# Kernel optimization log

Measured on AMD Instinct MI355X. Metric: run time of the kernel, lower is better.

## Reference

```python
import jax, jax.numpy as jnp
import numpy as np

B, T, C, H = 4, 1024, 512, 8
HD = C // H
N_NODE, F_DIM, TOTAL_DIM = 64, 8, 16
SCALE = 1.0 / np.sqrt(HD)


def _build_mask():
    # causal tril with every (total_dim-1 mod total_dim)-th COLUMN zeroed
    m = np.tril(np.ones((T, T), dtype=np.float32))
    m[:, TOTAL_DIM - 1::TOTAL_DIM] = 0.0
    return jnp.asarray(m)

MASK = _build_mask()  # (T, T), 1 = keep, 0 = mask


def setup_inputs() -> dict:
    key = jax.random.key(0)
    ks = jax.random.split(key, 12)
    s = 0.02
    return {
        "x": jax.random.normal(ks[0], (B, T, C), dtype=jnp.float32),
        "attn_bias": jax.random.normal(ks[1], (H, N_NODE, N_NODE), dtype=jnp.float32) * 0.1,
        "Wq": jax.random.normal(ks[2], (C, C), dtype=jnp.float32) * s,
        "bq": jax.random.normal(ks[3], (C,), dtype=jnp.float32) * s,
        "Wk": jax.random.normal(ks[4], (C, C), dtype=jnp.float32) * s,
        "bk": jax.random.normal(ks[5], (C,), dtype=jnp.float32) * s,
        "Wv": jax.random.normal(ks[6], (C, C), dtype=jnp.float32) * s,
        "bv": jax.random.normal(ks[7], (C,), dtype=jnp.float32) * s,
        "Wp": jax.random.normal(ks[8], (C, C), dtype=jnp.float32) * s,
        "bp": jax.random.normal(ks[9], (C,), dtype=jnp.float32) * s,
    }


def reference(x, attn_bias, Wq, bq, Wk, bk, Wv, bv, Wp, bp):
    Bx, Tx, Cx = x.shape

    def heads(W, b):  # (B,T,C) -> (B,H,T,HD); torch Linear is x @ W.T + b
        return (x @ W.T + b).reshape(Bx, Tx, H, HD).transpose(0, 2, 1, 3)

    q, k, v = heads(Wq, bq), heads(Wk, bk), heads(Wv, bv)

    # repeat_interleave + repeat expansion == kron(attn_bias, ones(f_dim, f_dim))
    d = N_NODE * F_DIM
    bias = jnp.repeat(jnp.repeat(attn_bias, F_DIM, axis=1), F_DIM, axis=2)  # (H, d, d)
    padded_bias = jnp.zeros((H, Tx, Tx), dtype=x.dtype).at[:, :d, :d].set(bias)

    att = jnp.einsum('bhqd,bhkd->bhqk', q, k) * SCALE + padded_bias[None]
    neg = jnp.asarray(-jnp.inf, dtype=att.dtype)
    att = jnp.where(MASK[None, None, :Tx, :Tx] == 0, neg, att)
    att = jax.nn.softmax(att, axis=-1)

    y = jnp.einsum('bhqk,bhkd->bhqd', att, v)
    y = y.transpose(0, 2, 1, 3).reshape(Bx, Tx, Cx)
    return y @ Wp.T + bp
```

## Files before the change

### kernel.cpp

```cpp
#include <hip/hip_runtime.h>

#define T_SEQ 1024
#define C_DIM 512
#define H_HEADS 8
#define HDIM 64
#define B_BATCH 4
#define M_ROWS (B_BATCH * T_SEQ)
#define NSPLIT_TOT 40

typedef __attribute__((ext_vector_type(8))) short short8;
typedef __attribute__((ext_vector_type(4))) float f32x4;

__device__ __forceinline__ unsigned short f2bf(float f) {
    unsigned u = __builtin_bit_cast(unsigned, f);
    u += 0x7FFFu + ((u >> 16) & 1u);
    return (unsigned short)(u >> 16);
}

__device__ __forceinline__ float bf2f(unsigned short u) {
    return __builtin_bit_cast(float, (unsigned)u << 16);
}

__device__ __forceinline__ void gload_lds16(const unsigned short* g, unsigned short* l) {
    __builtin_amdgcn_global_load_lds(
        (const __attribute__((address_space(1))) unsigned int*)(const void*)g,
        (__attribute__((address_space(3))) unsigned int*)(void*)l, 16, 0, 0);
}

__device__ __constant__ unsigned char BX_OF[NSPLIT_TOT] =
    {0,1,2,3,4,4,5,5,6,6,7,7,8,8,8,9,9,9,10,10,10,11,11,11,
     12,12,12,12,13,13,13,13,14,14,14,14,15,15,15,15};
__device__ __constant__ unsigned char SP_OF[NSPLIT_TOT] =
    {0,0,0,0,0,1,0,1,0,1,0,1,0,1,2,0,1,2,0,1,2,0,1,2,
     0,1,2,3,0,1,2,3,0,1,2,3,0,1,2,3};
__device__ __constant__ unsigned char CUM_OF[16] =
    {0,1,2,3,4,6,8,10,12,15,18,21,24,28,32,36};

__global__ __launch_bounds__(256) void cast_all(
    const float* __restrict__ x,
    const float* __restrict__ wq, const float* __restrict__ wk,
    const float* __restrict__ wv, const float* __restrict__ wp,
    unsigned short* __restrict__ xb,
    unsigned short* __restrict__ wqb, unsigned short* __restrict__ wkb,
    unsigned short* __restrict__ wvb, unsigned short* __restrict__ wpb)
{
    const long NX = (long)M_ROWS * C_DIM;
    const long NW = (long)C_DIM * C_DIM;
    long i4 = (long)blockIdx.x * blockDim.x + threadIdx.x;
    long base = i4 * 4;
    const float* src; unsigned short* dst; long off;
    if (base < NX) { src = x; dst = xb; off = base; }
    else {
        long r = base - NX;
        int w = (int)(r >> 18);
        off = r & (NW - 1);
        switch (w) {
            case 0:  src = wq; dst = wqb; break;
            case 1:  src = wk; dst = wkb; break;
            case 2:  src = wv; dst = wvb; break;
            default: src = wp; dst = wpb; break;
        }
    }
    float4 v = *(const float4*)(src + off);
    ushort4 o;
    o.x = f2bf(v.x); o.y = f2bf(v.y); o.z = f2bf(v.z); o.w = f2bf(v.w);
    *(ushort4*)(dst + off) = o;
}

__device__ __forceinline__ void gemm_body(
    const unsigned short* __restrict__ A,
    const unsigned short* __restrict__ W,
    const float* __restrict__ bias,
    unsigned short* __restrict__ Obf,
    float* __restrict__ Of,
    int mode)
{
    __shared__ __align__(16) unsigned short Atile[2][128 * 64];
    __shared__ __align__(16) unsigned short Btile[2][64 * 64];

    const int tid  = threadIdx.x;
    const int w    = tid >> 6;
    const int lane = tid & 63;
    const int quad = lane >> 4;
    const int l16  = lane & 15;
    const int m0   = blockIdx.x * 128;
    const int n0   = blockIdx.y * 64;

    f32x4 acc[2][4] = {};

    const int lr = lane >> 3;
    const int lc = lane & 7;

    auto stage = [&](int buf, int kk) {
        for (int i = 0; i < 4; ++i) {
            int r0 = 32 * w + 8 * i;
            int r  = r0 + lr;
            int c  = lc ^ (r & 7);
            gload_lds16(&A[(long)(m0 + r) * 512 + kk + c * 8], &Atile[buf][r0 * 64]);
        }
        for (int i = 0; i < 2; ++i) {
            int r0 = 16 * w + 8 * i;
            int r  = r0 + lr;
            int c  = lc ^ (r & 7);
            gload_lds16(&W[(long)(n0 + r) * 512 + kk + c * 8], &Btile[buf][r0 * 64]);
        }
    };

    stage(0, 0);

    #pragma unroll
    for (int k0 = 0; k0 < 512; k0 += 64) {
        const int cur = (k0 >> 6) & 1;
        if (k0 + 64 < 512) {
            __builtin_amdgcn_sched_barrier(0);
            stage(cur ^ 1, k0 + 64);
            asm volatile("s_waitcnt vmcnt(6)" ::: "memory");
        } else {
            asm volatile("s_waitcnt vmcnt(0)" ::: "memory");
        }
        __builtin_amdgcn_s_barrier();
        __builtin_amdgcn_sched_barrier(0);

        for (int st = 0; st < 2; ++st) {
            const int pc = ((4 * st + quad) ^ (l16 & 7)) * 8;
            short8 af[2], bf[4];
            for (int i = 0; i < 2; ++i)
                af[i] = *(const short8*)&Atile[cur][(32 * w + 16 * i + l16) * 64 + pc];
            for (int j = 0; j < 4; ++j)
                bf[j] = *(const short8*)&Btile[cur][(16 * j + l16) * 64 + pc];
            for (int i = 0; i < 2; ++i)
                for (int j = 0; j < 4; ++j)
                    acc[i][j] = (mode == 1)
                        ? __builtin_amdgcn_mfma_f32_16x16x32_bf16(bf[j], af[i], acc[i][j], 0, 0, 0)
                        : __builtin_amdgcn_mfma_f32_16x16x32_bf16(af[i], bf[j], acc[i][j], 0, 0, 0);
        }

        __builtin_amdgcn_sched_barrier(0);
        __builtin_amdgcn_s_barrier();
    }

    if (mode == 1) {
        for (int j = 0; j < 4; ++j) {
            for (int reg = 0; reg < 4; ++reg) {
                int n = n0 + 16 * j + 4 * quad + reg;
                int h = n >> 6, hd = n & 63;
                float bv = bias[n];
                for (int i = 0; i < 2; ++i) {
                    int t = m0 + 32 * w + 16 * i + l16;
                    int b = t >> 10, tl = t & 1023;
                    Obf[(((long)(b * H_HEADS + h)) * HDIM + hd) * T_SEQ + tl] =
                        f2bf(acc[i][j][reg] + bv);
                }
            }
        }
    } else {
        for (int j = 0; j < 4; ++j) {
            int col = n0 + 16 * j + l16;
            float bv = bias[col];
            for (int i = 0; i < 2; ++i) {
                for (int reg = 0; reg < 4; ++reg) {
                    int row = m0 + 32 * w + 16 * i + 4 * quad + reg;
                    float v = acc[i][j][reg] + bv;
                    if (mode == 2) {
                        Of[(long)row * 512 + col] = v;
                    } else {
                        int b = row >> 10, t = row & 1023;
                        int h = col >> 6,  hd = col & 63;
                        Obf[(((long)(b * H_HEADS + h)) * T_SEQ + t) * HDIM + hd] = f2bf(v);
                    }
                }
            }
        }
    }
}

__global__ __launch_bounds__(256) void gemm_qkv(
    const unsigned short* __restrict__ A,
    const unsigned short* __restrict__ Wq, const unsigned short* __restrict__ Wk,
    const unsigned short* __restrict__ Wv,
    const float* __restrict__ bq, const float* __restrict__ bk, const float* __restrict__ bv,
    unsigned short* __restrict__ Q, unsigned short* __restrict__ K,
    unsigned short* __restrict__ V)
{
    const unsigned short* W; const float* b; unsigned short* O; int mode;
    if (blockIdx.z == 0)      { W = Wq; b = bq; O = Q; mode = 0; }
    else if (blockIdx.z == 1) { W = Wk; b = bk; O = K; mode = 0; }
    else                      { W = Wv; b = bv; O = V; mode = 1; }
    gemm_body(A, W, b, O, nullptr, mode);
}

__global__ __launch_bounds__(256) void gemm_out_k(
    const unsigned short* __restrict__ A, const unsigned short* __restrict__ W,
    const float* __restrict__ bias, float* __restrict__ O)
{
    gemm_body(A, W, bias, nullptr, O, 2);
}

__global__ __launch_bounds__(256, 5) void attn_split(
    const unsigned short* __restrict__ Q, const unsigned short* __restrict__ K,
    const unsigned short* __restrict__ Vt, const float* __restrict__ attn_bias,
    unsigned short* __restrict__ Opart, float* __restrict__ lpart)
{
    __shared__ __align__(16) unsigned short Kl[64 * 64];
    __shared__ __align__(16) unsigned short Vl[64 * 64];
    __shared__ __align__(16) unsigned short Pl[4][16 * 72];
    __shared__ float biasl[8][64];

    const int tid  = threadIdx.x;
    const int w    = tid >> 6;
    const int lane = tid & 63;
    const int quad = lane >> 4;
    const int l16  = lane & 15;
    const int lr   = lane >> 3;
    const int lc   = lane & 7;
    const int sidx = blockIdx.y;
    const int bh   = blockIdx.x;
    const int h    = bh & 7;
    const int bx   = BX_OF[sidx];
    const int sp   = SP_OF[sidx];
    const int q0   = bx * 64;
    const int kt0  = sp * 4;
    const int kt1  = min(kt0 + 4, bx + 1);
    const bool use_bias = (q0 < 512) && (sp < 2);

    const int qrow  = q0 + 16 * w + l16;
    const int brow2 = 2 * w + (l16 >> 3);

    if (use_bias) {
        for (int i = tid; i < 512; i += 256) {
            int nq = (q0 >> 3) + (i >> 6);
            biasl[i >> 6][i & 63] = attn_bias[h * 4096 + nq * 64 + (i & 63)];
        }
    }

    const unsigned short* Qbh = Q  + (long)bh * T_SEQ * HDIM;
    const unsigned short* Kbh = K  + (long)bh * T_SEQ * HDIM;
    const unsigned short* Vbh = Vt + (long)bh * HDIM * T_SEQ;

    short8 qf[2];
    {
        qf[0] = *(const short8*)&Qbh[(long)qrow * HDIM + 8 * quad];
        qf[1] = *(const short8*)&Qbh[(long)qrow * HDIM + 32 + 8 * quad];
    }

    f32x4 oacc[4] = {};
    float lsum = 0.f;

    for (int kt = kt0; kt < kt1; ++kt) {
        const int k0 = kt * 64;
        __syncthreads();
        for (int i = 0; i < 2; ++i) {
            int r0 = 16 * w + 8 * i;
            int r  = r0 + lr;
            int c  = lc ^ (r & 7);
            gload_lds16(&Kbh[(long)(k0 + r) * HDIM + c * 8], &Kl[r0 * 64]);
            gload_lds16(&Vbh[(long)r * T_SEQ + k0 + c * 8], &Vl[r0 * 64]);
        }
        __syncthreads();

        f32x4 s[4] = {};
        __builtin_amdgcn_s_setprio(1);
        for (int st = 0; st < 2; ++st) {
            const int pc = ((4 * st + quad) ^ (l16 & 7)) * 8;
            for (int ct = 0; ct < 4; ++ct) {
                short8 kf = *(const short8*)&Kl[(16 * ct + l16) * 64 + pc];
                s[ct] = __builtin_amdgcn_mfma_f32_16x16x32_bf16(kf, qf[st], s[ct], 0, 0, 0);
            }
        }
        __builtin_amdgcn_s_setprio(0);

        const bool diag = (kt == bx);
        #pragma unroll
        for (int ct = 0; ct < 4; ++ct) {
            const int kbase = k0 + 16 * ct + 4 * quad;
            float bval = use_bias ? biasl[brow2][(k0 >> 3) + 2 * ct + (quad >> 1)] : 0.f;
            float pv[4];
            #pragma unroll
            for (int reg = 0; reg < 4; ++reg) {
                float v = s[ct][reg] * 0.125f + bval;
                bool keep = !(quad == 3 && reg == 3);
                if (diag) keep = keep && (kbase + reg <= qrow);
                float p = keep ? __expf(v) : 0.f;
                lsum += p;
                pv[reg] = p;
            }
            uint2 d;
            d.x = (unsigned)f2bf(pv[0]) | ((unsigned)f2bf(pv[1]) << 16);
            d.y = (unsigned)f2bf(pv[2]) | ((unsigned)f2bf(pv[3]) << 16);
            *(uint2*)&Pl[w][l16 * 72 + 16 * ct + 4 * quad] = d;
        }

        __builtin_amdgcn_s_setprio(1);
        for (int st = 0; st < 2; ++st) {
            const int pc = ((4 * st + quad) ^ (l16 & 7)) * 8;
            short8 af = *(const short8*)&Pl[w][l16 * 72 + 32 * st + 8 * quad];
            for (int ct = 0; ct < 4; ++ct) {
                short8 bf = *(const short8*)&Vl[(16 * ct + l16) * 64 + pc];
                oacc[ct] = __builtin_amdgcn_mfma_f32_16x16x32_bf16(af, bf, oacc[ct], 0, 0, 0);
            }
        }
        __builtin_amdgcn_s_setprio(0);
    }

    lsum += __shfl_xor(lsum, 16);
    lsum += __shfl_xor(lsum, 32);

    const long p = (long)bh * NSPLIT_TOT + sidx;
    unsigned short* Op = Opart + p * 4096;
    for (int ct = 0; ct < 4; ++ct)
        for (int reg = 0; reg < 4; ++reg)
            Op[(16 * w + 4 * quad + reg) * 64 + 16 * ct + l16] = f2bf(oacc[ct][reg]);
    if (quad == 0)
        lpart[p * 64 + 16 * w + l16] = lsum;
}

__global__ __launch_bounds__(256) void attn_combine(
    const unsigned short* __restrict__ Opart, const float* __restrict__ lpart,
    unsigned short* __restrict__ Y)
{
    const int bx = blockIdx.y, bh = blockIdx.x;
    const int b = bh >> 3, h = bh & 7;
    const int ns = (bx >> 2) + 1;
    const long p0 = (long)bh * NSPLIT_TOT + CUM_OF[bx];
    const int tid = threadIdx.x;
    const int qr = tid >> 2;
    const int hs = (tid & 3) * 16;

    float L = 0.f;
    for (int s = 0; s < ns; ++s) L += lpart[(p0 + s) * 64 + qr];

    float acc[16] = {};
    for (int s = 0; s < ns; ++s) {
        const unsigned short* op = Opart + (p0 + s) * 4096 + qr * 64 + hs;
        short8 v0 = *(const short8*)op;
        short8 v1 = *(const short8*)(op + 8);
        for (int k = 0; k < 8; ++k) {
            acc[k]     += bf2f((unsigned short)v0[k]);
            acc[k + 8] += bf2f((unsigned short)v1[k]);
        }
    }
    float inv = 1.f / L;
    int q = bx * 64 + qr;
    unsigned short* y = Y + ((long)b * T_SEQ + q) * C_DIM + h * HDIM + hs;
    for (int j4 = 0; j4 < 4; ++j4) {
        ushort4 o;
        o.x = f2bf(acc[4 * j4 + 0] * inv); o.y = f2bf(acc[4 * j4 + 1] * inv);
        o.z = f2bf(acc[4 * j4 + 2] * inv); o.w = f2bf(acc[4 * j4 + 3] * inv);
        *(ushort4*)(y + 4 * j4) = o;
    }
}

extern "C" void kernel_launch(void* const* d_in, const int* in_sizes, int n_in,
                              void* d_out, int out_size, void* d_ws, size_t ws_size,
                              hipStream_t stream)
{
    const float* x         = (const float*)d_in[0];
    const float* attn_bias = (const float*)d_in[1];
    const float* Wq = (const float*)d_in[2]; const float* bq = (const float*)d_in[3];
    const float* Wk = (const float*)d_in[4]; const float* bk = (const float*)d_in[5];
    const float* Wv = (const float*)d_in[6]; const float* bv = (const float*)d_in[7];
    const float* Wp = (const float*)d_in[8]; const float* bp = (const float*)d_in[9];
    float* out = (float*)d_out;

    const long NX = (long)M_ROWS * C_DIM;
    const long NW = (long)C_DIM * C_DIM;

    unsigned short* xb  = (unsigned short*)d_ws;
    unsigned short* wqb = xb  + NX;
    unsigned short* wkb = wqb + NW;
    unsigned short* wvb = wkb + NW;
    unsigned short* wpb = wvb + NW;
    unsigned short* Qb  = wpb + NW;
    unsigned short* Kb  = Qb  + NX;
    unsigned short* Vtb = Kb  + NX;
    unsigned short* Yb  = Vtb + NX;
    unsigned short* Opart = Yb + NX;
    float* lpart = (float*)(Opart + (long)32 * NSPLIT_TOT * 4096);

    long n4 = (NX + 4 * NW) / 4;
    cast_all<<<dim3((unsigned)(n4 / 256)), 256, 0, stream>>>(
        x, Wq, Wk, Wv, Wp, xb, wqb, wkb, wvb, wpb);

    gemm_qkv<<<dim3(M_ROWS / 128, C_DIM / 64, 3), 256, 0, stream>>>(
        xb, wqb, wkb, wvb, bq, bk, bv, Qb, Kb, Vtb);

    attn_split<<<dim3(B_BATCH * H_HEADS, NSPLIT_TOT), 256, 0, stream>>>(
        Qb, Kb, Vtb, attn_bias, Opart, lpart);

    attn_combine<<<dim3(B_BATCH * H_HEADS, T_SEQ / 64), 256, 0, stream>>>(
        Opart, lpart, Yb);

    gemm_out_k<<<dim3(M_ROWS / 128, C_DIM / 64), 256, 0, stream>>>(
        Yb, wpb, bp, out);
}
```

Before: 122.1 us.

## Enlarge attention query tile to 128 rows to reuse K/V tiles

The split attention kernel now processes 128 query rows per block (two 16-row subtiles per wave) instead of 64. Each K/V tile loaded into LDS therefore feeds twice as many MFMAs, and there are half as many split blocks. The split table, partial-output layout and combine indexing are rewritten to match. In exchange, register and LDS use per block rise (occupancy hint drops from 5 to 4 blocks), the grid shrinks to 640 blocks, and the diagonal masking now covers two key tiles.

```diff
diff --git a/kernel.cpp b/kernel.cpp
--- a/kernel.cpp
+++ b/kernel.cpp
@@ -6,7 +6,7 @@
 #define HDIM 64
 #define B_BATCH 4
 #define M_ROWS (B_BATCH * T_SEQ)
-#define NSPLIT_TOT 40
+#define NSPLIT8 20
 
 typedef __attribute__((ext_vector_type(8))) short short8;
 typedef __attribute__((ext_vector_type(4))) float f32x4;
@@ -27,14 +27,12 @@
         (__attribute__((address_space(3))) unsigned int*)(void*)l, 16, 0, 0);
 }
 
-__device__ __constant__ unsigned char BX_OF[NSPLIT_TOT] =
-    {0,1,2,3,4,4,5,5,6,6,7,7,8,8,8,9,9,9,10,10,10,11,11,11,
-     12,12,12,12,13,13,13,13,14,14,14,14,15,15,15,15};
-__device__ __constant__ unsigned char SP_OF[NSPLIT_TOT] =
-    {0,0,0,0,0,1,0,1,0,1,0,1,0,1,2,0,1,2,0,1,2,0,1,2,
-     0,1,2,3,0,1,2,3,0,1,2,3,0,1,2,3};
-__device__ __constant__ unsigned char CUM_OF[16] =
-    {0,1,2,3,4,6,8,10,12,15,18,21,24,28,32,36};
+__device__ __constant__ unsigned char BX8_OF[NSPLIT8] =
+    {0,1,2,2,3,3,4,4,4,5,5,5,6,6,6,6,7,7,7,7};
+__device__ __constant__ unsigned char SP8_OF[NSPLIT8] =
+    {0,0,0,1,0,1,0,1,2,0,1,2,0,1,2,3,0,1,2,3};
+__device__ __constant__ unsigned char CUM8_OF[8] =
+    {0,1,2,4,6,9,12,16};
 
 __global__ __launch_bounds__(256) void cast_all(
     const float* __restrict__ x,
@@ -196,15 +194,15 @@
     gemm_body(A, W, bias, nullptr, O, 2);
 }
 
-__global__ __launch_bounds__(256, 5) void attn_split(
+__global__ __launch_bounds__(256, 4) void attn_split(
     const unsigned short* __restrict__ Q, const unsigned short* __restrict__ K,
     const unsigned short* __restrict__ Vt, const float* __restrict__ attn_bias,
     unsigned short* __restrict__ Opart, float* __restrict__ lpart)
 {
     __shared__ __align__(16) unsigned short Kl[64 * 64];
     __shared__ __align__(16) unsigned short Vl[64 * 64];
-    __shared__ __align__(16) unsigned short Pl[4][16 * 72];
-    __shared__ float biasl[8][64];
+    __shared__ __align__(16) unsigned short Pl[4][32 * 72];
+    __shared__ float biasl[16][64];
 
     const int tid  = threadIdx.x;
     const int w    = tid >> 6;
@@ -216,18 +214,16 @@
     const int sidx = blockIdx.y;
     const int bh   = blockIdx.x;
     const int h    = bh & 7;
-    const int bx   = BX_OF[sidx];
-    const int sp   = SP_OF[sidx];
-    const int q0   = bx * 64;
-    const int kt0  = sp * 4;
-    const int kt1  = min(kt0 + 4, bx + 1);
-    const bool use_bias = (q0 < 512) && (sp < 2);
-
-    const int qrow  = q0 + 16 * w + l16;
-    const int brow2 = 2 * w + (l16 >> 3);
+    const int bx8  = BX8_OF[sidx];
+    const int sp   = SP8_OF[sidx];
+    const int q0   = bx8 * 128;
+    const int nk   = 2 * bx8 + 2;
+    const int kt0  = 4 * sp;
+    const int kt1  = min(kt0 + 4, nk);
+    const bool use_bias = (bx8 < 4);
 
     if (use_bias) {
-        for (int i = tid; i < 512; i += 256) {
+        for (int i = tid; i < 1024; i += 256) {
             int nq = (q0 >> 3) + (i >> 6);
             biasl[i >> 6][i & 63] = attn_bias[h * 4096 + nq * 64 + (i & 63)];
         }
@@ -237,20 +233,23 @@
     const unsigned short* Kbh = K  + (long)bh * T_SEQ * HDIM;
     const unsigned short* Vbh = Vt + (long)bh * HDIM * T_SEQ;
 
-    short8 qf[2];
-    {
-        qf[0] = *(const short8*)&Qbh[(long)qrow * HDIM + 8 * quad];
-        qf[1] = *(const short8*)&Qbh[(long)qrow * HDIM + 32 + 8 * quad];
-    }
-
-    f32x4 oacc[4] = {};
-    float lsum = 0.f;
+    short8 qf[2][2];
+    int qrow[2];
+    #pragma unroll
+    for (int i = 0; i < 2; ++i) {
+        qrow[i] = q0 + 32 * w + 16 * i + l16;
+        qf[i][0] = *(const short8*)&Qbh[(long)qrow[i] * HDIM + 8 * quad];
+        qf[i][1] = *(const short8*)&Qbh[(long)qrow[i] * HDIM + 32 + 8 * quad];
+    }
+
+    f32x4 oacc[2][4] = {};
+    float lsum[2] = {0.f, 0.f};
 
     for (int kt = kt0; kt < kt1; ++kt) {
         const int k0 = kt * 64;
         __syncthreads();
-        for (int i = 0; i < 2; ++i) {
-            int r0 = 16 * w + 8 * i;
+        for (int i2 = 0; i2 < 2; ++i2) {
+            int r0 = 16 * w + 8 * i2;
             int r  = r0 + lr;
             int c  = lc ^ (r & 7);
             gload_lds16(&Kbh[(long)(k0 + r) * HDIM + c * 8], &Kl[r0 * 64]);
@@ -258,80 +257,104 @@
         }
         __syncthreads();
 
-        f32x4 s[4] = {};
+        f32x4 s[2][4] = {};
         __builtin_amdgcn_s_setprio(1);
         for (int st = 0; st < 2; ++st) {
             const int pc = ((4 * st + quad) ^ (l16 & 7)) * 8;
             for (int ct = 0; ct < 4; ++ct) {
                 short8 kf = *(const short8*)&Kl[(16 * ct + l16) * 64 + pc];
-                s[ct] = __builtin_amdgcn_mfma_f32_16x16x32_bf16(kf, qf[st], s[ct], 0, 0, 0);
+                s[0][ct] = __builtin_amdgcn_mfma_f32_16x16x32_bf16(kf, qf[0][st], s[0][ct], 0, 0, 0);
+                s[1][ct] = __builtin_amdgcn_mfma_f32_16x16x32_bf16(kf, qf[1][st], s[1][ct], 0, 0, 0);
             }
         }
         __builtin_amdgcn_s_setprio(0);
 
-        const bool diag = (kt == bx);
+        const bool diag = (kt >= 2 * bx8);
         #pragma unroll
-        for (int ct = 0; ct < 4; ++ct) {
-            const int kbase = k0 + 16 * ct + 4 * quad;
-            float bval = use_bias ? biasl[brow2][(k0 >> 3) + 2 * ct + (quad >> 1)] : 0.f;
-            float pv[4];
+        for (int i = 0; i < 2; ++i) {
             #pragma unroll
-            for (int reg = 0; reg < 4; ++reg) {
-                float v = s[ct][reg] * 0.125f + bval;
-                bool keep = !(quad == 3 && reg == 3);
-                if (diag) keep = keep && (kbase + reg <= qrow);
-                float p = keep ? __expf(v) : 0.f;
-                lsum += p;
-                pv[reg] = p;
+            for (int ct = 0; ct < 4; ++ct) {
+                const int kbase = k0 + 16 * ct + 4 * quad;
+                float bval = use_bias
+                    ? biasl[4 * w + 2 * i + (l16 >> 3)][(k0 >> 3) + 2 * ct + (quad >> 1)]
+                    : 0.f;
+                float pv[4];
+                #pragma unroll
+                for (int reg = 0; reg < 4; ++reg) {
+                    float v = fmaf(s[i][ct][reg], 0.125f, bval);
+                    bool keep = !(quad == 3 && reg == 3);
+                    if (diag) keep = keep && (kbase + reg <= qrow[i]);
+                    float p = keep ? __expf(v) : 0.f;
+                    lsum[i] += p;
+                    pv[reg] = p;
+                }
+                uint2 d;
+                d.x = (unsigned)f2bf(pv[0]) | ((unsigned)f2bf(pv[1]) << 16);
+                d.y = (unsigned)f2bf(pv[2]) | ((unsigned)f2bf(pv[3]) << 16);
+                *(uint2*)&Pl[w][(16 * i + l16) * 72 + 16 * ct + 4 * quad] = d;
             }
-            uint2 d;
-            d.x = (unsigned)f2bf(pv[0]) | ((unsigned)f2bf(pv[1]) << 16);
-            d.y = (unsigned)f2bf(pv[2]) | ((unsigned)f2bf(pv[3]) << 16);
-            *(uint2*)&Pl[w][l16 * 72 + 16 * ct + 4 * quad] = d;
         }
 
         __builtin_amdgcn_s_setprio(1);
         for (int st = 0; st < 2; ++st) {
             const int pc = ((4 * st + quad) ^ (l16 & 7)) * 8;
-            short8 af = *(const short8*)&Pl[w][l16 * 72 + 32 * st + 8 * quad];
-            for (int ct = 0; ct < 4; ++ct) {
-                short8 bf = *(const short8*)&Vl[(16 * ct + l16) * 64 + pc];
-                oacc[ct] = __builtin_amdgcn_mfma_f32_16x16x32_bf16(af, bf, oacc[ct], 0, 0, 0);
+            short8 vf[4];
+            #pragma unroll
+            for (int ct = 0; ct < 4; ++ct)
+                vf[ct] = *(const short8*)&Vl[(16 * ct + l16) * 64 + pc];
+            #pragma unroll
+            for (int i = 0; i < 2; ++i) {
+                short8 af = *(const short8*)&Pl[w][(16 * i + l16) * 72 + 32 * st + 8 * quad];
+                #pragma unroll
+                for (int ct = 0; ct < 4; ++ct)
+                    oacc[i][ct] = __builtin_amdgcn_mfma_f32_16x16x32_bf16(af, vf[ct], oacc[i][ct], 0, 0, 0);
             }
         }
         __builtin_amdgcn_s_setprio(0);
     }
 
-    lsum += __shfl_xor(lsum, 16);
-    lsum += __shfl_xor(lsum, 32);
-
-    const long p = (long)bh * NSPLIT_TOT + sidx;
-    unsigned short* Op = Opart + p * 4096;
-    for (int ct = 0; ct < 4; ++ct)
-        for (int reg = 0; reg < 4; ++reg)
-            Op[(16 * w + 4 * quad + reg) * 64 + 16 * ct + l16] = f2bf(oacc[ct][reg]);
-    if (quad == 0)
-        lpart[p * 64 + 16 * w + l16] = lsum;
+    #pragma unroll
+    for (int i = 0; i < 2; ++i) {
+        lsum[i] += __shfl_xor(lsum[i], 16);
+        lsum[i] += __shfl_xor(lsum[i], 32);
+    }
+
+    const long p = (long)bh * NSPLIT8 + sidx;
+    unsigned short* Op = Opart + p * 8192;
+    #pragma unroll
+    for (int i = 0; i < 2; ++i)
+        for (int ct = 0; ct < 4; ++ct)
+            for (int reg = 0; reg < 4; ++reg)
+                Op[(32 * w + 16 * i + 4 * quad + reg) * 64 + 16 * ct + l16] =
+                    f2bf(oacc[i][ct][reg]);
+    if (quad == 0) {
+        lpart[p * 128 + 32 * w + l16]      = lsum[0];
+        lpart[p * 128 + 32 * w + 16 + l16] = lsum[1];
+    }
 }
 
 __global__ __launch_bounds__(256) void attn_combine(
     const unsigned short* __restrict__ Opart, const float* __restrict__ lpart,
     unsigned short* __restrict__ Y)
 {
-    const int bx = blockIdx.y, bh = blockIdx.x;
+    const int bxc = blockIdx.y;
+    const int bh  = blockIdx.x;
     const int b = bh >> 3, h = bh & 7;
-    const int ns = (bx >> 2) + 1;
-    const long p0 = (long)bh * NSPLIT_TOT + CUM_OF[bx];
+    const int bx8  = bxc >> 1;
+    const int half = bxc & 1;
+    const int ns   = (bx8 >> 1) + 1;
+    const long p0  = (long)bh * NSPLIT8 + CUM8_OF[bx8];
     const int tid = threadIdx.x;
-    const int qr = tid >> 2;
-    const int hs = (tid & 3) * 16;
+    const int qr  = tid >> 2;
+    const int hs  = (tid & 3) * 16;
+    const int qloc = 64 * half + qr;
 
     float L = 0.f;
-    for (int s = 0; s < ns; ++s) L += lpart[(p0 + s) * 64 + qr];
+    for (int s = 0; s < ns; ++s) L += lpart[(p0 + s) * 128 + qloc];
 
     float acc[16] = {};
     for (int s = 0; s < ns; ++s) {
-        const unsigned short* op = Opart + (p0 + s) * 4096 + qr * 64 + hs;
+        const unsigned short* op = Opart + (p0 + s) * 8192 + qloc * 64 + hs;
         short8 v0 = *(const short8*)op;
         short8 v1 = *(const short8*)(op + 8);
         for (int k = 0; k < 8; ++k) {
@@ -340,7 +363,7 @@
         }
     }
     float inv = 1.f / L;
-    int q = bx * 64 + qr;
+    int q = bxc * 64 + qr;
     unsigned short* y = Y + ((long)b * T_SEQ + q) * C_DIM + h * HDIM + hs;
     for (int j4 = 0; j4 < 4; ++j4) {
         ushort4 o;
@@ -375,7 +398,7 @@
     unsigned short* Vtb = Kb  + NX;
     unsigned short* Yb  = Vtb + NX;
     unsigned short* Opart = Yb + NX;
-    float* lpart = (float*)(Opart + (long)32 * NSPLIT_TOT * 4096);
+    float* lpart = (float*)(Opart + (long)32 * NSPLIT8 * 8192);
 
     long n4 = (NX + 4 * NW) / 4;
     cast_all<<<dim3((unsigned)(n4 / 256)), 256, 0, stream>>>(
@@ -384,7 +407,7 @@
     gemm_qkv<<<dim3(M_ROWS / 128, C_DIM / 64, 3), 256, 0, stream>>>(
         xb, wqb, wkb, wvb, bq, bk, bv, Qb, Kb, Vtb);
 
-    attn_split<<<dim3(B_BATCH * H_HEADS, NSPLIT_TOT), 256, 0, stream>>>(
+    attn_split<<<dim3(B_BATCH * H_HEADS, NSPLIT8), 256, 0, stream>>>(
         Qb, Kb, Vtb, attn_bias, Opart, lpart);
 
     attn_combine<<<dim3(B_BATCH * H_HEADS, T_SEQ / 64), 256, 0, stream>>>(
```

Measured after the change: 123.3 us. No clear change (+1.0%).

## Fuse split attention and combine into one kernel with paired causal tiles

Applied to the files above, without the earlier changes.

Replaces the split-KV attention kernel and its separate combine kernel with one fused kernel. Each block handles two query tiles (pj and 15-pj), so every block walks 17 key tiles and the causal triangle is load-balanced. K/V tiles are double-buffered in LDS with asynchronous global-to-LDS loads and explicit waitcnt and barriers, so the next tile loads while the current one is computed. Normalized output goes straight to Y, which removes the partial-output and row-sum round trip and one kernel launch. The cost is far fewer blocks (256) and a long serial loop per block, so parallelism and latency hiding drop.

```diff
diff --git a/kernel.cpp b/kernel.cpp
--- a/kernel.cpp
+++ b/kernel.cpp
@@ -6,7 +6,6 @@
 #define HDIM 64
 #define B_BATCH 4
 #define M_ROWS (B_BATCH * T_SEQ)
-#define NSPLIT_TOT 40
 
 typedef __attribute__((ext_vector_type(8))) short short8;
 typedef __attribute__((ext_vector_type(4))) float f32x4;
@@ -26,15 +25,6 @@
         (const __attribute__((address_space(1))) unsigned int*)(const void*)g,
         (__attribute__((address_space(3))) unsigned int*)(void*)l, 16, 0, 0);
 }
-
-__device__ __constant__ unsigned char BX_OF[NSPLIT_TOT] =
-    {0,1,2,3,4,4,5,5,6,6,7,7,8,8,8,9,9,9,10,10,10,11,11,11,
-     12,12,12,12,13,13,13,13,14,14,14,14,15,15,15,15};
-__device__ __constant__ unsigned char SP_OF[NSPLIT_TOT] =
-    {0,0,0,0,0,1,0,1,0,1,0,1,0,1,2,0,1,2,0,1,2,0,1,2,
-     0,1,2,3,0,1,2,3,0,1,2,3,0,1,2,3};
-__device__ __constant__ unsigned char CUM_OF[16] =
-    {0,1,2,3,4,6,8,10,12,15,18,21,24,28,32,36};
 
 __global__ __launch_bounds__(256) void cast_all(
     const float* __restrict__ x,
@@ -196,13 +186,13 @@
     gemm_body(A, W, bias, nullptr, O, 2);
 }
 
-__global__ __launch_bounds__(256, 5) void attn_split(
+__global__ __launch_bounds__(256) void attn_fused(
     const unsigned short* __restrict__ Q, const unsigned short* __restrict__ K,
     const unsigned short* __restrict__ Vt, const float* __restrict__ attn_bias,
-    unsigned short* __restrict__ Opart, float* __restrict__ lpart)
-{
-    __shared__ __align__(16) unsigned short Kl[64 * 64];
-    __shared__ __align__(16) unsigned short Vl[64 * 64];
+    unsigned short* __restrict__ Y)
+{
+    __shared__ __align__(16) unsigned short Kl[2][64 * 64];
+    __shared__ __align__(16) unsigned short Vl[2][64 * 64];
     __shared__ __align__(16) unsigned short Pl[4][16 * 72];
     __shared__ float biasl[8][64];
 
@@ -213,71 +203,95 @@
     const int l16  = lane & 15;
     const int lr   = lane >> 3;
     const int lc   = lane & 7;
-    const int sidx = blockIdx.y;
     const int bh   = blockIdx.x;
+    const int pj   = blockIdx.y;
     const int h    = bh & 7;
-    const int bx   = BX_OF[sidx];
-    const int sp   = SP_OF[sidx];
-    const int q0   = bx * 64;
-    const int kt0  = sp * 4;
-    const int kt1  = min(kt0 + 4, bx + 1);
-    const bool use_bias = (q0 < 512) && (sp < 2);
-
-    const int qrow  = q0 + 16 * w + l16;
-    const int brow2 = 2 * w + (l16 >> 3);
-
-    if (use_bias) {
-        for (int i = tid; i < 512; i += 256) {
-            int nq = (q0 >> 3) + (i >> 6);
-            biasl[i >> 6][i & 63] = attn_bias[h * 4096 + nq * 64 + (i & 63)];
-        }
+    const int b    = bh >> 3;
+
+    const int q0A = pj * 64;
+    const int q0B = (15 - pj) * 64;
+    const int nA  = pj + 1;
+    const int nT  = 17;
+
+    for (int i = tid; i < 512; i += 256) {
+        int nq = (q0A >> 3) + (i >> 6);
+        biasl[i >> 6][i & 63] = attn_bias[h * 4096 + nq * 64 + (i & 63)];
     }
 
     const unsigned short* Qbh = Q  + (long)bh * T_SEQ * HDIM;
     const unsigned short* Kbh = K  + (long)bh * T_SEQ * HDIM;
     const unsigned short* Vbh = Vt + (long)bh * HDIM * T_SEQ;
 
-    short8 qf[2];
-    {
-        qf[0] = *(const short8*)&Qbh[(long)qrow * HDIM + 8 * quad];
-        qf[1] = *(const short8*)&Qbh[(long)qrow * HDIM + 32 + 8 * quad];
-    }
-
+    const int qrowA = q0A + 16 * w + l16;
+    const int qrowB = q0B + 16 * w + l16;
+    short8 qfA0 = *(const short8*)&Qbh[(long)qrowA * HDIM + 8 * quad];
+    short8 qfA1 = *(const short8*)&Qbh[(long)qrowA * HDIM + 32 + 8 * quad];
+    short8 qfB0 = *(const short8*)&Qbh[(long)qrowB * HDIM + 8 * quad];
+    short8 qfB1 = *(const short8*)&Qbh[(long)qrowB * HDIM + 32 + 8 * quad];
+
+    auto stage = [&](int buf, int k0) {
+        for (int i2 = 0; i2 < 2; ++i2) {
+            int r0 = 16 * w + 8 * i2;
+            int r  = r0 + lr;
+            int c  = lc ^ (r & 7);
+            gload_lds16(&Kbh[(long)(k0 + r) * HDIM + c * 8], &Kl[buf][r0 * 64]);
+            gload_lds16(&Vbh[(long)r * T_SEQ + k0 + c * 8], &Vl[buf][r0 * 64]);
+        }
+    };
+
+    const int brow2 = 2 * w + (l16 >> 3);
+
+    short8 qf0 = qfA0, qf1 = qfA1;
+    int qrow = qrowA, q0c = q0A;
+    bool phB = false;
     f32x4 oacc[4] = {};
     float lsum = 0.f;
 
-    for (int kt = kt0; kt < kt1; ++kt) {
+    stage(0, 0);
+
+    for (int t = 0; t < nT; ++t) {
+        const int cur = t & 1;
+        if (t == nA) {
+            qf0 = qfB0; qf1 = qfB1; qrow = qrowB; q0c = q0B; phB = true;
+            for (int ct = 0; ct < 4; ++ct) oacc[ct] = f32x4{};
+            lsum = 0.f;
+        }
+        const int kt = phB ? (t - nA) : t;
         const int k0 = kt * 64;
-        __syncthreads();
-        for (int i = 0; i < 2; ++i) {
-            int r0 = 16 * w + 8 * i;
-            int r  = r0 + lr;
-            int c  = lc ^ (r & 7);
-            gload_lds16(&Kbh[(long)(k0 + r) * HDIM + c * 8], &Kl[r0 * 64]);
-            gload_lds16(&Vbh[(long)r * T_SEQ + k0 + c * 8], &Vl[r0 * 64]);
-        }
-        __syncthreads();
+
+        if (t + 1 < nT) {
+            __builtin_amdgcn_sched_barrier(0);
+            const int t2 = t + 1;
+            const int k0n = ((t2 < nA) ? t2 : (t2 - nA)) * 64;
+            stage(cur ^ 1, k0n);
+            asm volatile("s_waitcnt vmcnt(4)" ::: "memory");
+        } else {
+            asm volatile("s_waitcnt vmcnt(0)" ::: "memory");
+        }
+        __builtin_amdgcn_s_barrier();
+        __builtin_amdgcn_sched_barrier(0);
 
         f32x4 s[4] = {};
         __builtin_amdgcn_s_setprio(1);
         for (int st = 0; st < 2; ++st) {
             const int pc = ((4 * st + quad) ^ (l16 & 7)) * 8;
+            short8 qf = st ? qf1 : qf0;
             for (int ct = 0; ct < 4; ++ct) {
-                short8 kf = *(const short8*)&Kl[(16 * ct + l16) * 64 + pc];
-                s[ct] = __builtin_amdgcn_mfma_f32_16x16x32_bf16(kf, qf[st], s[ct], 0, 0, 0);
+                short8 kf = *(const short8*)&Kl[cur][(16 * ct + l16) * 64 + pc];
+                s[ct] = __builtin_amdgcn_mfma_f32_16x16x32_bf16(kf, qf, s[ct], 0, 0, 0);
             }
         }
         __builtin_amdgcn_s_setprio(0);
 
-        const bool diag = (kt == bx);
+        const bool diag = (t == nA - 1) || (t == nT - 1);
         #pragma unroll
         for (int ct = 0; ct < 4; ++ct) {
             const int kbase = k0 + 16 * ct + 4 * quad;
-            float bval = use_bias ? biasl[brow2][(k0 >> 3) + 2 * ct + (quad >> 1)] : 0.f;
+            float bval = !phB ? biasl[brow2][(k0 >> 3) + 2 * ct + (quad >> 1)] : 0.f;
             float pv[4];
             #pragma unroll
             for (int reg = 0; reg < 4; ++reg) {
-                float v = s[ct][reg] * 0.125f + bval;
+                float v = fmaf(s[ct][reg], 0.125f, bval);
                 bool keep = !(quad == 3 && reg == 3);
                 if (diag) keep = keep && (kbase + reg <= qrow);
                 float p = keep ? __expf(v) : 0.f;
@@ -295,58 +309,32 @@
             const int pc = ((4 * st + quad) ^ (l16 & 7)) * 8;
             short8 af = *(const short8*)&Pl[w][l16 * 72 + 32 * st + 8 * quad];
             for (int ct = 0; ct < 4; ++ct) {
-                short8 bf = *(const short8*)&Vl[(16 * ct + l16) * 64 + pc];
-                oacc[ct] = __builtin_amdgcn_mfma_f32_16x16x32_bf16(af, bf, oacc[ct], 0, 0, 0);
+                short8 vf = *(const short8*)&Vl[cur][(16 * ct + l16) * 64 + pc];
+                oacc[ct] = __builtin_amdgcn_mfma_f32_16x16x32_bf16(af, vf, oacc[ct], 0, 0, 0);
             }
         }
         __builtin_amdgcn_s_setprio(0);
-    }
-
-    lsum += __shfl_xor(lsum, 16);
-    lsum += __shfl_xor(lsum, 32);
-
-    const long p = (long)bh * NSPLIT_TOT + sidx;
-    unsigned short* Op = Opart + p * 4096;
-    for (int ct = 0; ct < 4; ++ct)
-        for (int reg = 0; reg < 4; ++reg)
-            Op[(16 * w + 4 * quad + reg) * 64 + 16 * ct + l16] = f2bf(oacc[ct][reg]);
-    if (quad == 0)
-        lpart[p * 64 + 16 * w + l16] = lsum;
-}
-
-__global__ __launch_bounds__(256) void attn_combine(
-    const unsigned short* __restrict__ Opart, const float* __restrict__ lpart,
-    unsigned short* __restrict__ Y)
-{
-    const int bx = blockIdx.y, bh = blockIdx.x;
-    const int b = bh >> 3, h = bh & 7;
-    const int ns = (bx >> 2) + 1;
-    const long p0 = (long)bh * NSPLIT_TOT + CUM_OF[bx];
-    const int tid = threadIdx.x;
-    const int qr = tid >> 2;
-    const int hs = (tid & 3) * 16;
-
-    float L = 0.f;
-    for (int s = 0; s < ns; ++s) L += lpart[(p0 + s) * 64 + qr];
-
-    float acc[16] = {};
-    for (int s = 0; s < ns; ++s) {
-        const unsigned short* op = Opart + (p0 + s) * 4096 + qr * 64 + hs;
-        short8 v0 = *(const short8*)op;
-        short8 v1 = *(const short8*)(op + 8);
-        for (int k = 0; k < 8; ++k) {
-            acc[k]     += bf2f((unsigned short)v0[k]);
-            acc[k + 8] += bf2f((unsigned short)v1[k]);
-        }
-    }
-    float inv = 1.f / L;
-    int q = bx * 64 + qr;
-    unsigned short* y = Y + ((long)b * T_SEQ + q) * C_DIM + h * HDIM + hs;
-    for (int j4 = 0; j4 < 4; ++j4) {
-        ushort4 o;
-        o.x = f2bf(acc[4 * j4 + 0] * inv); o.y = f2bf(acc[4 * j4 + 1] * inv);
-        o.z = f2bf(acc[4 * j4 + 2] * inv); o.w = f2bf(acc[4 * j4 + 3] * inv);
-        *(ushort4*)(y + 4 * j4) = o;
+
+        __builtin_amdgcn_sched_barrier(0);
+        __builtin_amdgcn_s_barrier();
+
+        if (diag) {
+            float ls = lsum;
+            ls += __shfl_xor(ls, 16);
+            ls += __shfl_xor(ls, 32);
+            float linv[4];
+            #pragma unroll
+            for (int reg = 0; reg < 4; ++reg)
+                linv[reg] = 1.f / __shfl(ls, 4 * quad + reg);
+            #pragma unroll
+            for (int ct = 0; ct < 4; ++ct)
+                #pragma unroll
+                for (int reg = 0; reg < 4; ++reg) {
+                    int q = q0c + 16 * w + 4 * quad + reg;
+                    Y[((long)b * T_SEQ + q) * C_DIM + h * HDIM + 16 * ct + l16] =
+                        f2bf(oacc[ct][reg] * linv[reg]);
+                }
+        }
     }
 }
 
@@ -374,8 +362,6 @@
     unsigned short* Kb  = Qb  + NX;
     unsigned short* Vtb = Kb  + NX;
     unsigned short* Yb  = Vtb + NX;
-    unsigned short* Opart = Yb + NX;
-    float* lpart = (float*)(Opart + (long)32 * NSPLIT_TOT * 4096);
 
     long n4 = (NX + 4 * NW) / 4;
     cast_all<<<dim3((unsigned)(n4 / 256)), 256, 0, stream>>>(
@@ -384,11 +370,8 @@
     gemm_qkv<<<dim3(M_ROWS / 128, C_DIM / 64, 3), 256, 0, stream>>>(
         xb, wqb, wkb, wvb, bq, bk, bv, Qb, Kb, Vtb);
 
-    attn_split<<<dim3(B_BATCH * H_HEADS, NSPLIT_TOT), 256, 0, stream>>>(
-        Qb, Kb, Vtb, attn_bias, Opart, lpart);
-
-    attn_combine<<<dim3(B_BATCH * H_HEADS, T_SEQ / 64), 256, 0, stream>>>(
-        Opart, lpart, Yb);
+    attn_fused<<<dim3(B_BATCH * H_HEADS, 8), 256, 0, stream>>>(
+        Qb, Kb, Vtb, attn_bias, Yb);
 
     gemm_out_k<<<dim3(M_ROWS / 128, C_DIM / 64), 256, 0, stream>>>(
         Yb, wpb, bp, out);
```

After: 131.7 us. +7.9%, slower.
